# Kernel tuning notes

Hardware: AMD Instinct MI355X
Metric: run time of the kernel (lower is better)

Reference implementation:

```python
import jax, jax.numpy as jnp
import numpy as np

B, S, H = 2, 2048, 4096
NH, NKV, HD = 32, 8, 128
N_REP = NH // NKV
SCALING = HD ** -0.5


def rotate_half(x):
    x1, x2 = x[..., : HD // 2], x[..., HD // 2 :]
    return jnp.concatenate((-x2, x1), axis=-1)


def setup_inputs() -> dict:
    key = jax.random.key(0)
    ks = jax.random.split(key, 8)
    hidden_states = jax.random.normal(ks[0], (B, S, H), dtype=jnp.float32)
    # RoPE tables computed as in Llama (deterministic, realistic values)
    inv_freq = 1.0 / (10000.0 ** (jnp.arange(0, HD, 2, dtype=jnp.float32) / HD))
    t = jnp.arange(S, dtype=jnp.float32)
    freqs = jnp.einsum('s,d->sd', t, inv_freq)
    emb = jnp.concatenate((freqs, freqs), axis=-1)  # [S, HD]
    cos = jnp.broadcast_to(jnp.cos(emb)[None], (B, S, HD))
    sin = jnp.broadcast_to(jnp.sin(emb)[None], (B, S, HD))
    # additive causal mask [B,1,S,S]
    causal = jnp.where(jnp.tril(jnp.ones((S, S), dtype=bool)), 0.0, -1e9).astype(jnp.float32)
    attention_mask = jnp.broadcast_to(causal[None, None], (B, 1, S, S))
    std = 0.02
    Wq = jax.random.normal(ks[1], (NH * HD, H), dtype=jnp.float32) * std
    Wk = jax.random.normal(ks[2], (NKV * HD, H), dtype=jnp.float32) * std
    Wv = jax.random.normal(ks[3], (NKV * HD, H), dtype=jnp.float32) * std
    Wo = jax.random.normal(ks[4], (H, NH * HD), dtype=jnp.float32) * std
    return dict(hidden_states=hidden_states, cos=cos, sin=sin,
                attention_mask=attention_mask, Wq=Wq, Wk=Wk, Wv=Wv, Wo=Wo)


def reference(hidden_states, cos, sin, attention_mask, Wq, Wk, Wv, Wo):
    b, s, _ = hidden_states.shape
    # projections (torch Linear: x @ W.T), split into heads -> [B, nH, S, HD]
    q = (hidden_states @ Wq.T).reshape(b, s, NH, HD).transpose(0, 2, 1, 3)
    k = (hidden_states @ Wk.T).reshape(b, s, NKV, HD).transpose(0, 2, 1, 3)
    v = (hidden_states @ Wv.T).reshape(b, s, NKV, HD).transpose(0, 2, 1, 3)
    # RoPE: cos/sin [B,S,HD] -> [B,1,S,HD]
    c, sn = cos[:, None], sin[:, None]
    q = q * c + rotate_half(q) * sn
    k = k * c + rotate_half(k) * sn
    # GQA: repeat kv heads
    k = jnp.repeat(k, N_REP, axis=1)
    v = jnp.repeat(v, N_REP, axis=1)
    scores = jnp.einsum('bhqd,bhkd->bhqk', q, k) * SCALING + attention_mask
    attn = jax.nn.softmax(scores.astype(jnp.float32), axis=-1).astype(q.dtype)
    out = jnp.einsum('bhqk,bhkd->bhqd', attn, v)
    out = out.transpose(0, 2, 1, 3).reshape(b, s, NH * HD)
    return out @ Wo.T
```

## Files before the change

### kernel.cpp

```cpp
#include <hip/hip_runtime.h>
#include <stdint.h>

typedef unsigned short u16;
typedef __attribute__((ext_vector_type(8))) short short8;
typedef __attribute__((ext_vector_type(4))) float f32x4;
typedef __attribute__((ext_vector_type(16))) float f32x16;
typedef __attribute__((ext_vector_type(4))) u16 u16x4;

static constexpr float SCALE = 0.08838834764831845f;
static constexpr float QSCALE = 0.12752459769642898f;

__device__ __forceinline__ u16 f2bf(float f) {
    union { float f; unsigned u; } x; x.f = f;
    unsigned r = x.u + 0x7fffu + ((x.u >> 16) & 1u);
    return (u16)(r >> 16);
}
__device__ __forceinline__ float bf2f(u16 b) {
    union { unsigned u; float f; } x; x.u = ((unsigned)b) << 16;
    return x.f;
}
__device__ __forceinline__ unsigned cvt_pk_bf16(float lo, float hi_) {
    unsigned r;
    asm("v_cvt_pk_bf16_f32 %0, %1, %2" : "=v"(r) : "v"(lo), "v"(hi_));
    return r;
}

__global__ __launch_bounds__(256) void convert5_kernel(const float* __restrict__ s0, const float* __restrict__ s1,
                                                       const float* __restrict__ s2, const float* __restrict__ s3,
                                                       const float* __restrict__ s4,
                                                       u16* __restrict__ d0, u16* __restrict__ d1,
                                                       u16* __restrict__ d2, u16* __restrict__ d3,
                                                       u16* __restrict__ d4) {
    const int V0 = 4194304, V1 = 8388608, V2 = 9437184, V3 = 10485760, V4 = 14680064;
    const int stride = gridDim.x * blockDim.x;
    for (int i = blockIdx.x * blockDim.x + threadIdx.x; i < V4; i += stride) {
        const float* sp; u16* dp; int off;
        if (i < V0)      { sp = s0; dp = d0; off = i; }
        else if (i < V1) { sp = s1; dp = d1; off = i - V0; }
        else if (i < V2) { sp = s2; dp = d2; off = i - V1; }
        else if (i < V3) { sp = s3; dp = d3; off = i - V2; }
        else             { sp = s4; dp = d4; off = i - V3; }
        float4 v = *reinterpret_cast<const float4*>(sp + (size_t)off * 4);
        u16x4 o;
        o.x = f2bf(v.x); o.y = f2bf(v.y); o.z = f2bf(v.z); o.w = f2bf(v.w);
        *reinterpret_cast<u16x4*>(dp + (size_t)off * 4) = o;
    }
}

__global__ __launch_bounds__(256) void gemm_kv(const u16* __restrict__ A,
                                               const u16* __restrict__ Bk,
                                               const u16* __restrict__ Bv,
                                               u16* __restrict__ Ck,
                                               u16* __restrict__ Cvt) {
    constexpr int K = 4096, N = 1024, BK = 64;
    __shared__ u16 sA[128 * BK];
    __shared__ u16 sB[128 * BK];
    const int tid = threadIdx.x;
    const int wid = tid >> 6, lane = tid & 63;
    const int lrow = lane & 15, lgrp = lane >> 4;

    int bid = blockIdx.x;
    { const int cpx = 512 >> 3; bid = (bid & 7) * cpx + (bid >> 3); }
    const bool isV = bid >= 256;
    const int b2 = bid & 255;
    const int row0 = (b2 >> 3) * 128, col0 = (b2 & 7) * 128;
    const u16* __restrict__ B = isV ? Bv : Bk;
    const int wr = (wid >> 1) * 64, wc = (wid & 1) * 64;

    f32x4 acc[4][4] = {};

    const int NT = K / BK;
    for (int kt = 0; kt < NT; ++kt) {
        const int k0 = kt * BK;
        __syncthreads();
        #pragma unroll
        for (int rnd = 0; rnd < 4; ++rnd) {
            const int eoff = (rnd * 256 + tid) * 8;
            const int r = eoff >> 6, c = eoff & 63;
            const int gc = c ^ ((r & 7) << 3);
            const int ldsoff = rnd * 2048 + wid * 512;
            __builtin_amdgcn_global_load_lds(
                (const __attribute__((address_space(1))) void*)(A + (size_t)(row0 + r) * K + k0 + gc),
                (__attribute__((address_space(3))) void*)(&sA[ldsoff]), 16, 0, 0);
            __builtin_amdgcn_global_load_lds(
                (const __attribute__((address_space(1))) void*)(B + (size_t)(col0 + r) * K + k0 + gc),
                (__attribute__((address_space(3))) void*)(&sB[ldsoff]), 16, 0, 0);
        }
        __syncthreads();
        #pragma unroll
        for (int kk = 0; kk < 2; ++kk) {
            const int koff = kk * 32 + lgrp * 8;
            short8 af[4], bfr[4];
            #pragma unroll
            for (int m = 0; m < 4; ++m) {
                const int rr = wr + m * 16 + lrow;
                af[m] = *(const short8*)&sA[rr * BK + (koff ^ ((rr & 7) << 3))];
            }
            #pragma unroll
            for (int n = 0; n < 4; ++n) {
                const int rr = wc + n * 16 + lrow;
                bfr[n] = *(const short8*)&sB[rr * BK + (koff ^ ((rr & 7) << 3))];
            }
            #pragma unroll
            for (int m = 0; m < 4; ++m)
                #pragma unroll
                for (int n = 0; n < 4; ++n)
                    acc[m][n] = __builtin_amdgcn_mfma_f32_16x16x32_bf16(af[m], bfr[n], acc[m][n], 0, 0, 0);
        }
    }

    const int orow = row0 + wr + lgrp * 4;
    const int ocol = col0 + wc + lrow;
    if (!isV) {
        #pragma unroll
        for (int m = 0; m < 4; ++m)
            #pragma unroll
            for (int n = 0; n < 4; ++n)
                #pragma unroll
                for (int r = 0; r < 4; ++r)
                    Ck[(size_t)(orow + m * 16 + r) * N + ocol + n * 16] = f2bf(acc[m][n][r]);
    } else {
        #pragma unroll
        for (int m = 0; m < 4; ++m)
            #pragma unroll
            for (int n = 0; n < 4; ++n) {
                u16x4 pk;
                pk.x = f2bf(acc[m][n][0]); pk.y = f2bf(acc[m][n][1]);
                pk.z = f2bf(acc[m][n][2]); pk.w = f2bf(acc[m][n][3]);
                *(u16x4*)&Cvt[(size_t)(ocol + n * 16) * 4096 + orow + m * 16] = pk;
            }
    }
}

template<int OUT_MODE>
__global__ __launch_bounds__(512, 2) void gemm256v3(const u16* __restrict__ A,
                                                    const u16* __restrict__ B,
                                                    void* __restrict__ Cv,
                                                    int M, int N, int K) {
    __shared__ u16 sA[2][2][256 * 32];
    __shared__ u16 sB[2][2][256 * 32];
    const int tid = threadIdx.x;
    const int wid = tid >> 6, lane = tid & 63;
    const int lrow = lane & 15, lgrp = lane >> 4;

    const int nbn = N >> 8;
    const int total = (M >> 8) * nbn;
    int bid = blockIdx.x;
    if ((total & 7) == 0) { const int cpx = total >> 3; bid = (bid & 7) * cpx + (bid >> 3); }
    const int row0 = (bid / nbn) * 256, col0 = (bid % nbn) * 256;
    const int wr = (wid >> 2) * 128, wc = (wid & 3) * 64;

    f32x4 acc[8][4] = {};

    const int rS0 = wid * 32 + (lane >> 2);
    const int uS = lane & 3;

    auto stageA = [&](int nb, int kt, int kkh) {
        const int k0 = kt * 64 + kkh * 32;
        #pragma unroll
        for (int g = 0; g < 2; ++g) {
            const int r = rS0 + g * 16;
            const int cs = k0 + ((uS ^ ((r >> 1) & 3)) << 3);
            __builtin_amdgcn_global_load_lds(
                (const __attribute__((address_space(1))) void*)(A + (size_t)(row0 + r) * K + cs),
                (__attribute__((address_space(3))) void*)(&sA[nb][kkh][(wid * 32 + g * 16) * 32]), 16, 0, 0);
        }
    };
    auto stageB = [&](int nb, int kt, int kkh) {
        const int k0 = kt * 64 + kkh * 32;
        #pragma unroll
        for (int g = 0; g < 2; ++g) {
            const int r = rS0 + g * 16;
            const int cs = k0 + ((uS ^ ((r >> 1) & 3)) << 3);
            __builtin_amdgcn_global_load_lds(
                (const __attribute__((address_space(1))) void*)(B + (size_t)(col0 + r) * K + cs),
                (__attribute__((address_space(3))) void*)(&sB[nb][kkh][(wid * 32 + g * 16) * 32]), 16, 0, 0);
        }
    };

    auto rdA = [&](int buf, int kkh, int fr) -> short8 {
        const int r = wr + fr * 16 + lrow;
        return *(const short8*)&sA[buf][kkh][r * 32 + ((lgrp ^ ((r >> 1) & 3)) << 3)];
    };
    auto rdB = [&](int buf, int kkh, int fc) -> short8 {
        const int r = wc + fc * 16 + lrow;
        return *(const short8*)&sB[buf][kkh][r * 32 + ((lgrp ^ ((r >> 1) & 3)) << 3)];
    };

    const int NK = K >> 6;
    stageA(0, 0, 0); stageB(0, 0, 0); stageA(0, 0, 1); stageB(0, 0, 1);
    asm volatile("s_waitcnt vmcnt(4)" ::: "memory");
    __builtin_amdgcn_s_barrier();
    __builtin_amdgcn_sched_barrier(0);

    for (int kt = 0; kt < NK; ++kt) {
        const int buf = kt & 1, nb = buf ^ 1;
        const bool st = (kt + 1 < NK);
        short8 a[4], b[4], a2[4];

        #pragma unroll
        for (int fr = 0; fr < 4; ++fr) a[fr] = rdA(buf, 0, fr);
        #pragma unroll
        for (int fc = 0; fc < 4; ++fc) b[fc] = rdB(buf, 0, fc);
        if (st) stageA(nb, kt + 1, 0);
        asm volatile("s_waitcnt lgkmcnt(0)" ::: "memory");
        __builtin_amdgcn_sched_barrier(0);
        __builtin_amdgcn_s_setprio(1);
        #pragma unroll
        for (int fr = 0; fr < 4; ++fr)
            #pragma unroll
            for (int fc = 0; fc < 4; ++fc)
                acc[fr][fc] = __builtin_amdgcn_mfma_f32_16x16x32_bf16(a[fr], b[fc], acc[fr][fc], 0, 0, 0);
        __builtin_amdgcn_s_setprio(0);

        #pragma unroll
        for (int fr = 0; fr < 4; ++fr) a2[fr] = rdA(buf, 0, fr + 4);
        if (st) stageB(nb, kt + 1, 0);
        asm volatile("s_waitcnt lgkmcnt(0)" ::: "memory");
        __builtin_amdgcn_sched_barrier(0);
        __builtin_amdgcn_s_setprio(1);
        #pragma unroll
        for (int fr = 0; fr < 4; ++fr)
            #pragma unroll
            for (int fc = 0; fc < 4; ++fc)
                acc[fr + 4][fc] = __builtin_amdgcn_mfma_f32_16x16x32_bf16(a2[fr], b[fc], acc[fr + 4][fc], 0, 0, 0);
        __builtin_amdgcn_s_setprio(0);
        if (st) { asm volatile("s_waitcnt vmcnt(4)" ::: "memory"); }
        else    { asm volatile("s_waitcnt vmcnt(0)" ::: "memory"); }
        __builtin_amdgcn_s_barrier();
        __builtin_amdgcn_sched_barrier(0);

        #pragma unroll
        for (int fr = 0; fr < 4; ++fr) a[fr] = rdA(buf, 1, fr);
        #pragma unroll
        for (int fc = 0; fc < 4; ++fc) b[fc] = rdB(buf, 1, fc);
        if (st) stageA(nb, kt + 1, 1);
        asm volatile("s_waitcnt lgkmcnt(0)" ::: "memory");
        __builtin_amdgcn_sched_barrier(0);
        __builtin_amdgcn_s_setprio(1);
        #pragma unroll
        for (int fr = 0; fr < 4; ++fr)
            #pragma unroll
            for (int fc = 0; fc < 4; ++fc)
                acc[fr][fc] = __builtin_amdgcn_mfma_f32_16x16x32_bf16(a[fr], b[fc], acc[fr][fc], 0, 0, 0);
        __builtin_amdgcn_s_setprio(0);

        #pragma unroll
        for (int fr = 0; fr < 4; ++fr) a2[fr] = rdA(buf, 1, fr + 4);
        if (st) stageB(nb, kt + 1, 1);
        asm volatile("s_waitcnt lgkmcnt(0)" ::: "memory");
        __builtin_amdgcn_sched_barrier(0);
        __builtin_amdgcn_s_setprio(1);
        #pragma unroll
        for (int fr = 0; fr < 4; ++fr)
            #pragma unroll
            for (int fc = 0; fc < 4; ++fc)
                acc[fr + 4][fc] = __builtin_amdgcn_mfma_f32_16x16x32_bf16(a2[fr], b[fc], acc[fr + 4][fc], 0, 0, 0);
        __builtin_amdgcn_s_setprio(0);
        if (st) { asm volatile("s_waitcnt vmcnt(4)" ::: "memory"); }
        __builtin_amdgcn_s_barrier();
        __builtin_amdgcn_sched_barrier(0);
    }

    const int orow = row0 + wr + lgrp * 4;
    const int ocol = col0 + wc + lrow;
    if (OUT_MODE == 2) {
        float* C = (float*)Cv;
        #pragma unroll
        for (int m = 0; m < 8; ++m)
            #pragma unroll
            for (int n = 0; n < 4; ++n)
                #pragma unroll
                for (int r = 0; r < 4; ++r)
                    C[(size_t)(orow + m * 16 + r) * N + ocol + n * 16] = acc[m][n][r];
    } else {
        u16* C = (u16*)Cv;
        #pragma unroll
        for (int m = 0; m < 8; ++m)
            #pragma unroll
            for (int n = 0; n < 4; ++n)
                #pragma unroll
                for (int r = 0; r < 4; ++r)
                    C[(size_t)(orow + m * 16 + r) * N + ocol + n * 16] = f2bf(acc[m][n][r]);
    }
}

template<int NHEADS>
__global__ __launch_bounds__(256) void rope_kernel(u16* __restrict__ X,
                                                   const float* __restrict__ cosb,
                                                   const float* __restrict__ sinb,
                                                   float scale) {
    constexpr int LH = (NHEADS == 32) ? 5 : 3;
    const int total = 2 * 2048 * NHEADS * 64;
    const int stride = gridDim.x * blockDim.x;
    for (int i = blockIdx.x * blockDim.x + threadIdx.x; i < total; i += stride) {
        const int d = i & 63;
        const int h = (i >> 6) & (NHEADS - 1);
        const int rs = i >> (6 + LH);
        const size_t base = (size_t)rs * (NHEADS * 128) + h * 128 + d;
        const float c = cosb[rs * 128 + d] * scale;
        const float sn = sinb[rs * 128 + d] * scale;
        const float x1 = bf2f(X[base]);
        const float x2 = bf2f(X[base + 64]);
        X[base] = f2bf(x1 * c - x2 * sn);
        X[base + 64] = f2bf(x2 * c + x1 * sn);
    }
}

__global__ __launch_bounds__(512, 2) void attn_kernel(const u16* __restrict__ Q,
                                                      const u16* __restrict__ K,
                                                      const u16* __restrict__ Vt,
                                                      u16* __restrict__ AO,
                                                      const float* __restrict__ cosp,
                                                      const float* __restrict__ sinp) {
    __shared__ u16 sK[2][64 * 128];
    __shared__ u16 sV[2][128 * 64];
    const int tid = threadIdx.x;
    const int wid = tid >> 6, lane = tid & 63;
    const int l31 = lane & 31, hi = lane >> 5;

    const int gg = blockIdx.x >> 6;
    const int bx = (gg < 4) ? gg : 11 - gg;
    const int rem = blockIdx.x & 63;
    const int h = rem >> 1;
    const int b = rem & 1;
    const int hkv = h >> 2;
    const int rs0 = b * 2048;
    const int q0 = bx * 256;
    const int qw = q0 + wid * 32;
    const int q_lane = qw + l31;

    short8 qf[8];
    {
        const u16* qb = Q + (size_t)(rs0 + q_lane) * 4096 + h * 128 + hi * 8;
        #pragma unroll
        for (int f = 0; f < 8; ++f) qf[f] = *(const short8*)(qb + f * 16);
        const float* cb = cosp + (size_t)(rs0 + q_lane) * 128 + hi * 8;
        const float* sb = sinp + (size_t)(rs0 + q_lane) * 128 + hi * 8;
        #pragma unroll
        for (int f = 0; f < 4; ++f) {
            float4 c0 = *(const float4*)(cb + f * 16);
            float4 c1 = *(const float4*)(cb + f * 16 + 4);
            float4 s0 = *(const float4*)(sb + f * 16);
            float4 s1 = *(const float4*)(sb + f * 16 + 4);
            const float cc[8] = {c0.x, c0.y, c0.z, c0.w, c1.x, c1.y, c1.z, c1.w};
            const float ss[8] = {s0.x, s0.y, s0.z, s0.w, s1.x, s1.y, s1.z, s1.w};
            #pragma unroll
            for (int jj = 0; jj < 8; ++jj) {
                const float x1 = bf2f((u16)qf[f][jj]);
                const float x2 = bf2f((u16)qf[f + 4][jj]);
                qf[f][jj]     = (short)f2bf((x1 * cc[jj] - x2 * ss[jj]) * QSCALE);
                qf[f + 4][jj] = (short)f2bf((x2 * cc[jj] + x1 * ss[jj]) * QSCALE);
            }
        }
    }

    f32x16 accO[4] = {};
    float m_c = -1e30f, l_c = 0.f;

    auto stage = [&](int bf, int t) {
        const int kv0 = t * 64;
        #pragma unroll
        for (int rnd = 0; rnd < 2; ++rnd) {
            {
                const int e = rnd * 4096 + tid * 8;
                const int r = e >> 7, c = e & 127;
                const int cs = c ^ ((r & 15) << 3);
                __builtin_amdgcn_global_load_lds(
                    (const __attribute__((address_space(1))) void*)(K + (size_t)(rs0 + kv0 + r) * 1024 + hkv * 128 + cs),
                    (__attribute__((address_space(3))) void*)(&sK[bf][rnd * 4096 + wid * 512]), 16, 0, 0);
            }
            {
                const int e = rnd * 4096 + tid * 8;
                const int r = e >> 6, c = e & 63;
                const int cs = c ^ ((r & 7) << 3);
                __builtin_amdgcn_global_load_lds(
                    (const __attribute__((address_space(1))) void*)(Vt + (size_t)(hkv * 128 + r) * 4096 + rs0 + kv0 + cs),
                    (__attribute__((address_space(3))) void*)(&sV[bf][rnd * 4096 + wid * 512]), 16, 0, 0);
            }
        }
    };

    const int NT = 4 * (bx + 1);
    stage(0, 0);
    __syncthreads();
    int buf = 0;

    for (int t = 0; t < NT; ++t) {
        if (t + 1 < NT) stage(buf ^ 1, t + 1);
        const int kv0 = t * 64;

        if (kv0 <= qw + 31) {
            f32x16 sc[2] = {};
            #pragma unroll
            for (int f = 0; f < 8; ++f) {
                const int col = f * 16 + hi * 8;
                const int r0 = l31, r1 = 32 + l31;
                short8 k0 = *(const short8*)&sK[buf][r0 * 128 + (col ^ ((r0 & 15) << 3))];
                short8 k1 = *(const short8*)&sK[buf][r1 * 128 + (col ^ ((r1 & 15) << 3))];
                sc[0] = __builtin_amdgcn_mfma_f32_32x32x16_bf16(k0, qf[f], sc[0], 0, 0, 0);
                sc[1] = __builtin_amdgcn_mfma_f32_32x32x16_bf16(k1, qf[f], sc[1], 0, 0, 0);
            }

            if (kv0 + 63 > q_lane) {
                #pragma unroll
                for (int blk = 0; blk < 2; ++blk)
                    #pragma unroll
                    for (int r = 0; r < 16; ++r) {
                        const int kv_abs = kv0 + blk * 32 + ((r & 3) + 8 * (r >> 2) + 4 * hi);
                        if (kv_abs > q_lane) sc[blk][r] = -1e30f;
                    }
            }

            float mx = sc[0][0];
            #pragma unroll
            for (int blk = 0; blk < 2; ++blk)
                #pragma unroll
                for (int r = 0; r < 16; ++r) mx = fmaxf(mx, sc[blk][r]);
            mx = fmaxf(mx, __shfl_xor(mx, 32));

            if (!__all(mx <= m_c + 8.0f)) {
                const float sclf = __builtin_amdgcn_exp2f(m_c - mx);
                m_c = mx;
                l_c *= sclf;
                float sclq[16];
                #pragma unroll
                for (int r = 0; r < 16; ++r)
                    sclq[r] = __shfl(sclf, (r & 3) + 8 * (r >> 2) + 4 * hi);
                #pragma unroll
                for (int d4 = 0; d4 < 4; ++d4)
                    #pragma unroll
                    for (int r = 0; r < 16; ++r) accO[d4][r] *= sclq[r];
            }
            float ssum = 0.f;
            #pragma unroll
            for (int blk = 0; blk < 2; ++blk)
                #pragma unroll
                for (int r = 0; r < 16; ++r) {
                    const float p = __builtin_amdgcn_exp2f(sc[blk][r] - m_c);
                    sc[blk][r] = p;
                    ssum += p;
                }
            ssum += __shfl_xor(ssum, 32);
            l_c += ssum;

            #pragma unroll
            for (int blk = 0; blk < 2; ++blk) {
                #pragma unroll
                for (int tt = 0; tt < 2; ++tt) {
                    const unsigned cv00 = cvt_pk_bf16(sc[blk][8 * tt + 0], sc[blk][8 * tt + 1]);
                    const unsigned cv01 = cvt_pk_bf16(sc[blk][8 * tt + 2], sc[blk][8 * tt + 3]);
                    const unsigned cv10 = cvt_pk_bf16(sc[blk][8 * tt + 4], sc[blk][8 * tt + 5]);
                    const unsigned cv11 = cvt_pk_bf16(sc[blk][8 * tt + 6], sc[blk][8 * tt + 7]);
                    const unsigned s00 = __shfl_xor(cv00, 32);
                    const unsigned s01 = __shfl_xor(cv01, 32);
                    const unsigned s10 = __shfl_xor(cv10, 32);
                    const unsigned s11 = __shfl_xor(cv11, 32);
                    union { unsigned w[4]; short8 v; } pa;
                    pa.w[0] = hi ? s10 : cv00;
                    pa.w[1] = hi ? s11 : cv01;
                    pa.w[2] = hi ? cv10 : s00;
                    pa.w[3] = hi ? cv11 : s01;
                    const int kvb = blk * 32 + tt * 16 + hi * 8;
                    #pragma unroll
                    for (int d4 = 0; d4 < 4; ++d4) {
                        const int vr = d4 * 32 + l31;
                        short8 vf = *(const short8*)&sV[buf][vr * 64 + (kvb ^ ((vr & 7) << 3))];
                        accO[d4] = __builtin_amdgcn_mfma_f32_32x32x16_bf16(pa.v, vf, accO[d4], 0, 0, 0);
                    }
                }
            }
        }
        __syncthreads();
        buf ^= 1;
    }

    const float invl = 1.0f / l_c;
    float invq[16];
    #pragma unroll
    for (int r = 0; r < 16; ++r)
        invq[r] = __shfl(invl, (r & 3) + 8 * (r >> 2) + 4 * hi);
    #pragma unroll
    for (int d4 = 0; d4 < 4; ++d4)
        #pragma unroll
        for (int r = 0; r < 16; ++r) {
            const int q = qw + (r & 3) + 8 * (r >> 2) + 4 * hi;
            AO[(size_t)(rs0 + q) * 4096 + h * 128 + d4 * 32 + l31] = f2bf(accO[d4][r] * invq[r]);
        }
}

extern "C" void kernel_launch(void* const* d_in, const int* in_sizes, int n_in,
                              void* d_out, int out_size, void* d_ws, size_t ws_size,
                              hipStream_t stream) {
    const float* hs   = (const float*)d_in[0];
    const float* cosp = (const float*)d_in[1];
    const float* sinp = (const float*)d_in[2];
    const float* Wq = (const float*)d_in[4];
    const float* Wk = (const float*)d_in[5];
    const float* Wv = (const float*)d_in[6];
    const float* Wo = (const float*)d_in[7];

    u16* Xb = (u16*)d_out;
    u16* Qb = (u16*)d_out + 16777216;
    char* w = (char*)d_ws;
    u16* Wqb = (u16*)w; w += 33554432;
    u16* Wkb = (u16*)w; w += 8388608;
    u16* Wvb = (u16*)w; w += 8388608;
    u16* Wob = (u16*)w; w += 33554432;
    u16* Kb  = (u16*)w; w += 8388608;
    u16* Vtb = (u16*)w; w += 8388608;
    u16* AOb = (u16*)w; w += 33554432;

    convert5_kernel<<<4096, 256, 0, stream>>>(hs, Wq, Wk, Wv, Wo, Xb, Wqb, Wkb, Wvb, Wob);

    gemm256v3<0><<<256, 512, 0, stream>>>(Xb, Wqb, Qb, 4096, 4096, 4096);
    gemm_kv<<<512, 256, 0, stream>>>(Xb, Wkb, Wvb, Kb, Vtb);

    rope_kernel<8><<<1024, 256, 0, stream>>>(Kb, cosp, sinp, 1.0f);

    attn_kernel<<<512, 512, 0, stream>>>(Qb, Kb, Vtb, AOb, cosp, sinp);

    gemm256v3<2><<<256, 512, 0, stream>>>(AOb, Wob, (float*)d_out, 4096, 4096, 4096);
}
```

Before: 523.8 us.

## Software-pipeline LDS fragment reads across MFMA phases in 256x256 GEMM

Restructures the GEMM main loop so the LDS fragment loads for the next MFMA block are issued before the current block's MFMAs run. Partial lgkmcnt waits let the matrix instructions overlap shared-memory reads, and the first fragments of the next k-tile are prefetched after the barrier. Launch bounds drop to one 512-thread block per CU so the extra fragment registers fit, at the cost of lower occupancy for the Q and output projections.

```diff
diff --git a/kernel.cpp b/kernel.cpp
--- a/kernel.cpp
+++ b/kernel.cpp
@@ -133,7 +133,7 @@
 }
 
 template<int OUT_MODE>
-__global__ __launch_bounds__(512, 2) void gemm256v3(const u16* __restrict__ A,
+__global__ __launch_bounds__(512, 1) void gemm256v5(const u16* __restrict__ A,
                                                     const u16* __restrict__ B,
                                                     void* __restrict__ Cv,
                                                     int M, int N, int K) {
@@ -193,72 +193,86 @@
     __builtin_amdgcn_s_barrier();
     __builtin_amdgcn_sched_barrier(0);
 
+    short8 a0[4], b0[4], a1[4], a2[4], b1[4], a3[4];
+    #pragma unroll
+    for (int fr = 0; fr < 4; ++fr) a0[fr] = rdA(0, 0, fr);
+    #pragma unroll
+    for (int fc = 0; fc < 4; ++fc) b0[fc] = rdB(0, 0, fc);
+    __builtin_amdgcn_sched_barrier(0);
+
     for (int kt = 0; kt < NK; ++kt) {
         const int buf = kt & 1, nb = buf ^ 1;
         const bool st = (kt + 1 < NK);
-        short8 a[4], b[4], a2[4];
-
-        #pragma unroll
-        for (int fr = 0; fr < 4; ++fr) a[fr] = rdA(buf, 0, fr);
-        #pragma unroll
-        for (int fc = 0; fc < 4; ++fc) b[fc] = rdB(buf, 0, fc);
+
+        #pragma unroll
+        for (int fr = 0; fr < 4; ++fr) a1[fr] = rdA(buf, 0, fr + 4);
         if (st) stageA(nb, kt + 1, 0);
-        asm volatile("s_waitcnt lgkmcnt(0)" ::: "memory");
+        asm volatile("s_waitcnt lgkmcnt(4)" ::: "memory");
         __builtin_amdgcn_sched_barrier(0);
         __builtin_amdgcn_s_setprio(1);
         #pragma unroll
         for (int fr = 0; fr < 4; ++fr)
             #pragma unroll
             for (int fc = 0; fc < 4; ++fc)
-                acc[fr][fc] = __builtin_amdgcn_mfma_f32_16x16x32_bf16(a[fr], b[fc], acc[fr][fc], 0, 0, 0);
+                acc[fr][fc] = __builtin_amdgcn_mfma_f32_16x16x32_bf16(a0[fr], b0[fc], acc[fr][fc], 0, 0, 0);
         __builtin_amdgcn_s_setprio(0);
-
-        #pragma unroll
-        for (int fr = 0; fr < 4; ++fr) a2[fr] = rdA(buf, 0, fr + 4);
+        __builtin_amdgcn_sched_barrier(0);
+
         if (st) stageB(nb, kt + 1, 0);
         asm volatile("s_waitcnt lgkmcnt(0)" ::: "memory");
         __builtin_amdgcn_sched_barrier(0);
-        __builtin_amdgcn_s_setprio(1);
-        #pragma unroll
-        for (int fr = 0; fr < 4; ++fr)
-            #pragma unroll
-            for (int fc = 0; fc < 4; ++fc)
-                acc[fr + 4][fc] = __builtin_amdgcn_mfma_f32_16x16x32_bf16(a2[fr], b[fc], acc[fr + 4][fc], 0, 0, 0);
-        __builtin_amdgcn_s_setprio(0);
         if (st) { asm volatile("s_waitcnt vmcnt(4)" ::: "memory"); }
         else    { asm volatile("s_waitcnt vmcnt(0)" ::: "memory"); }
         __builtin_amdgcn_s_barrier();
         __builtin_amdgcn_sched_barrier(0);
-
-        #pragma unroll
-        for (int fr = 0; fr < 4; ++fr) a[fr] = rdA(buf, 1, fr);
-        #pragma unroll
-        for (int fc = 0; fc < 4; ++fc) b[fc] = rdB(buf, 1, fc);
+        #pragma unroll
+        for (int fr = 0; fr < 4; ++fr) a2[fr] = rdA(buf, 1, fr);
+        #pragma unroll
+        for (int fc = 0; fc < 4; ++fc) b1[fc] = rdB(buf, 1, fc);
+        __builtin_amdgcn_sched_barrier(0);
+        __builtin_amdgcn_s_setprio(1);
+        #pragma unroll
+        for (int fr = 0; fr < 4; ++fr)
+            #pragma unroll
+            for (int fc = 0; fc < 4; ++fc)
+                acc[fr + 4][fc] = __builtin_amdgcn_mfma_f32_16x16x32_bf16(a1[fr], b0[fc], acc[fr + 4][fc], 0, 0, 0);
+        __builtin_amdgcn_s_setprio(0);
+        __builtin_amdgcn_sched_barrier(0);
+
+        #pragma unroll
+        for (int fr = 0; fr < 4; ++fr) a3[fr] = rdA(buf, 1, fr + 4);
         if (st) stageA(nb, kt + 1, 1);
-        asm volatile("s_waitcnt lgkmcnt(0)" ::: "memory");
+        asm volatile("s_waitcnt lgkmcnt(4)" ::: "memory");
         __builtin_amdgcn_sched_barrier(0);
         __builtin_amdgcn_s_setprio(1);
         #pragma unroll
         for (int fr = 0; fr < 4; ++fr)
             #pragma unroll
             for (int fc = 0; fc < 4; ++fc)
-                acc[fr][fc] = __builtin_amdgcn_mfma_f32_16x16x32_bf16(a[fr], b[fc], acc[fr][fc], 0, 0, 0);
+                acc[fr][fc] = __builtin_amdgcn_mfma_f32_16x16x32_bf16(a2[fr], b1[fc], acc[fr][fc], 0, 0, 0);
         __builtin_amdgcn_s_setprio(0);
-
-        #pragma unroll
-        for (int fr = 0; fr < 4; ++fr) a2[fr] = rdA(buf, 1, fr + 4);
+        __builtin_amdgcn_sched_barrier(0);
+
         if (st) stageB(nb, kt + 1, 1);
         asm volatile("s_waitcnt lgkmcnt(0)" ::: "memory");
         __builtin_amdgcn_sched_barrier(0);
-        __builtin_amdgcn_s_setprio(1);
-        #pragma unroll
-        for (int fr = 0; fr < 4; ++fr)
-            #pragma unroll
-            for (int fc = 0; fc < 4; ++fc)
-                acc[fr + 4][fc] = __builtin_amdgcn_mfma_f32_16x16x32_bf16(a2[fr], b[fc], acc[fr + 4][fc], 0, 0, 0);
-        __builtin_amdgcn_s_setprio(0);
         if (st) { asm volatile("s_waitcnt vmcnt(4)" ::: "memory"); }
         __builtin_amdgcn_s_barrier();
+        __builtin_amdgcn_sched_barrier(0);
+        if (st) {
+            #pragma unroll
+            for (int fr = 0; fr < 4; ++fr) a0[fr] = rdA(nb, 0, fr);
+            #pragma unroll
+            for (int fc = 0; fc < 4; ++fc) b0[fc] = rdB(nb, 0, fc);
+        }
+        __builtin_amdgcn_sched_barrier(0);
+        __builtin_amdgcn_s_setprio(1);
+        #pragma unroll
+        for (int fr = 0; fr < 4; ++fr)
+            #pragma unroll
+            for (int fc = 0; fc < 4; ++fc)
+                acc[fr + 4][fc] = __builtin_amdgcn_mfma_f32_16x16x32_bf16(a3[fr], b1[fc], acc[fr + 4][fc], 0, 0, 0);
+        __builtin_amdgcn_s_setprio(0);
         __builtin_amdgcn_sched_barrier(0);
     }
 
@@ -513,12 +527,12 @@
 
     convert5_kernel<<<4096, 256, 0, stream>>>(hs, Wq, Wk, Wv, Wo, Xb, Wqb, Wkb, Wvb, Wob);
 
-    gemm256v3<0><<<256, 512, 0, stream>>>(Xb, Wqb, Qb, 4096, 4096, 4096);
+    gemm256v5<0><<<256, 512, 0, stream>>>(Xb, Wqb, Qb, 4096, 4096, 4096);
     gemm_kv<<<512, 256, 0, stream>>>(Xb, Wkb, Wvb, Kb, Vtb);
 
     rope_kernel<8><<<1024, 256, 0, stream>>>(Kb, cosp, sinp, 1.0f);
 
     attn_kernel<<<512, 512, 0, stream>>>(Qb, Kb, Vtb, AOb, cosp, sinp);
 
-    gemm256v3<2><<<256, 512, 0, stream>>>(AOb, Wob, (float*)d_out, 4096, 4096, 4096);
-}
+    gemm256v5<2><<<256, 512, 0, stream>>>(AOb, Wob, (float*)d_out, 4096, 4096, 4096);
+}
```

New measurement: 502.4 us, median of 3. 1.04x faster.

## Rewrite 256x256 GEMM with 16 waves and a simpler double-buffered loop

Applied to the files above, without the earlier changes.

Replaces the 8-wave 256x256-tile GEMM with a 16-wave (1024-thread) variant. Each wave now owns a 64x64 subtile with a 4x4 accumulator instead of 128x64. The hand-scheduled interleaving of LDS reads, async global-to-LDS staging and explicit waitcnt is replaced by one stage-next-then-compute loop with a __syncthreads per k-step. The aim is more waves for latency hiding and less register pressure. The cost is losing the fine-grained overlap and the two-blocks-per-CU occupancy, and each wave reads more LDS per MFMA.

```diff
diff --git a/kernel.cpp b/kernel.cpp
--- a/kernel.cpp
+++ b/kernel.cpp
@@ -133,10 +133,10 @@
 }
 
 template<int OUT_MODE>
-__global__ __launch_bounds__(512, 2) void gemm256v3(const u16* __restrict__ A,
-                                                    const u16* __restrict__ B,
-                                                    void* __restrict__ Cv,
-                                                    int M, int N, int K) {
+__global__ __launch_bounds__(1024, 1) void gemm16w(const u16* __restrict__ A,
+                                                   const u16* __restrict__ B,
+                                                   void* __restrict__ Cv,
+                                                   int M, int N, int K) {
     __shared__ u16 sA[2][2][256 * 32];
     __shared__ u16 sB[2][2][256 * 32];
     const int tid = threadIdx.x;
@@ -148,118 +148,58 @@
     int bid = blockIdx.x;
     if ((total & 7) == 0) { const int cpx = total >> 3; bid = (bid & 7) * cpx + (bid >> 3); }
     const int row0 = (bid / nbn) * 256, col0 = (bid % nbn) * 256;
-    const int wr = (wid >> 2) * 128, wc = (wid & 3) * 64;
-
-    f32x4 acc[8][4] = {};
-
-    const int rS0 = wid * 32 + (lane >> 2);
-    const int uS = lane & 3;
-
-    auto stageA = [&](int nb, int kt, int kkh) {
-        const int k0 = kt * 64 + kkh * 32;
-        #pragma unroll
-        for (int g = 0; g < 2; ++g) {
-            const int r = rS0 + g * 16;
-            const int cs = k0 + ((uS ^ ((r >> 1) & 3)) << 3);
+    const int wr = (wid >> 2) * 64, wc = (wid & 3) * 64;
+
+    f32x4 acc[4][4] = {};
+
+    const int rS = tid >> 2;
+    const int uS = tid & 3;
+    const int sOff = wid * 512;
+
+    auto stage = [&](int nb, int kt) {
+        #pragma unroll
+        for (int kkh = 0; kkh < 2; ++kkh) {
+            const int k0 = kt * 64 + kkh * 32;
+            const int cs = k0 + ((uS ^ ((rS >> 1) & 3)) << 3);
             __builtin_amdgcn_global_load_lds(
-                (const __attribute__((address_space(1))) void*)(A + (size_t)(row0 + r) * K + cs),
-                (__attribute__((address_space(3))) void*)(&sA[nb][kkh][(wid * 32 + g * 16) * 32]), 16, 0, 0);
+                (const __attribute__((address_space(1))) void*)(A + (size_t)(row0 + rS) * K + cs),
+                (__attribute__((address_space(3))) void*)(&sA[nb][kkh][sOff]), 16, 0, 0);
+            __builtin_amdgcn_global_load_lds(
+                (const __attribute__((address_space(1))) void*)(B + (size_t)(col0 + rS) * K + cs),
+                (__attribute__((address_space(3))) void*)(&sB[nb][kkh][sOff]), 16, 0, 0);
         }
     };
-    auto stageB = [&](int nb, int kt, int kkh) {
-        const int k0 = kt * 64 + kkh * 32;
-        #pragma unroll
-        for (int g = 0; g < 2; ++g) {
-            const int r = rS0 + g * 16;
-            const int cs = k0 + ((uS ^ ((r >> 1) & 3)) << 3);
-            __builtin_amdgcn_global_load_lds(
-                (const __attribute__((address_space(1))) void*)(B + (size_t)(col0 + r) * K + cs),
-                (__attribute__((address_space(3))) void*)(&sB[nb][kkh][(wid * 32 + g * 16) * 32]), 16, 0, 0);
-        }
-    };
-
-    auto rdA = [&](int buf, int kkh, int fr) -> short8 {
-        const int r = wr + fr * 16 + lrow;
-        return *(const short8*)&sA[buf][kkh][r * 32 + ((lgrp ^ ((r >> 1) & 3)) << 3)];
-    };
-    auto rdB = [&](int buf, int kkh, int fc) -> short8 {
-        const int r = wc + fc * 16 + lrow;
-        return *(const short8*)&sB[buf][kkh][r * 32 + ((lgrp ^ ((r >> 1) & 3)) << 3)];
-    };
 
     const int NK = K >> 6;
-    stageA(0, 0, 0); stageB(0, 0, 0); stageA(0, 0, 1); stageB(0, 0, 1);
-    asm volatile("s_waitcnt vmcnt(4)" ::: "memory");
-    __builtin_amdgcn_s_barrier();
-    __builtin_amdgcn_sched_barrier(0);
+    stage(0, 0);
+    __syncthreads();
 
     for (int kt = 0; kt < NK; ++kt) {
-        const int buf = kt & 1, nb = buf ^ 1;
-        const bool st = (kt + 1 < NK);
-        short8 a[4], b[4], a2[4];
-
-        #pragma unroll
-        for (int fr = 0; fr < 4; ++fr) a[fr] = rdA(buf, 0, fr);
-        #pragma unroll
-        for (int fc = 0; fc < 4; ++fc) b[fc] = rdB(buf, 0, fc);
-        if (st) stageA(nb, kt + 1, 0);
-        asm volatile("s_waitcnt lgkmcnt(0)" ::: "memory");
-        __builtin_amdgcn_sched_barrier(0);
-        __builtin_amdgcn_s_setprio(1);
-        #pragma unroll
-        for (int fr = 0; fr < 4; ++fr)
-            #pragma unroll
-            for (int fc = 0; fc < 4; ++fc)
-                acc[fr][fc] = __builtin_amdgcn_mfma_f32_16x16x32_bf16(a[fr], b[fc], acc[fr][fc], 0, 0, 0);
-        __builtin_amdgcn_s_setprio(0);
-
-        #pragma unroll
-        for (int fr = 0; fr < 4; ++fr) a2[fr] = rdA(buf, 0, fr + 4);
-        if (st) stageB(nb, kt + 1, 0);
-        asm volatile("s_waitcnt lgkmcnt(0)" ::: "memory");
-        __builtin_amdgcn_sched_barrier(0);
-        __builtin_amdgcn_s_setprio(1);
-        #pragma unroll
-        for (int fr = 0; fr < 4; ++fr)
-            #pragma unroll
-            for (int fc = 0; fc < 4; ++fc)
-                acc[fr + 4][fc] = __builtin_amdgcn_mfma_f32_16x16x32_bf16(a2[fr], b[fc], acc[fr + 4][fc], 0, 0, 0);
-        __builtin_amdgcn_s_setprio(0);
-        if (st) { asm volatile("s_waitcnt vmcnt(4)" ::: "memory"); }
-        else    { asm volatile("s_waitcnt vmcnt(0)" ::: "memory"); }
-        __builtin_amdgcn_s_barrier();
-        __builtin_amdgcn_sched_barrier(0);
-
-        #pragma unroll
-        for (int fr = 0; fr < 4; ++fr) a[fr] = rdA(buf, 1, fr);
-        #pragma unroll
-        for (int fc = 0; fc < 4; ++fc) b[fc] = rdB(buf, 1, fc);
-        if (st) stageA(nb, kt + 1, 1);
-        asm volatile("s_waitcnt lgkmcnt(0)" ::: "memory");
-        __builtin_amdgcn_sched_barrier(0);
-        __builtin_amdgcn_s_setprio(1);
-        #pragma unroll
-        for (int fr = 0; fr < 4; ++fr)
-            #pragma unroll
-            for (int fc = 0; fc < 4; ++fc)
-                acc[fr][fc] = __builtin_amdgcn_mfma_f32_16x16x32_bf16(a[fr], b[fc], acc[fr][fc], 0, 0, 0);
-        __builtin_amdgcn_s_setprio(0);
-
-        #pragma unroll
-        for (int fr = 0; fr < 4; ++fr) a2[fr] = rdA(buf, 1, fr + 4);
-        if (st) stageB(nb, kt + 1, 1);
-        asm volatile("s_waitcnt lgkmcnt(0)" ::: "memory");
-        __builtin_amdgcn_sched_barrier(0);
-        __builtin_amdgcn_s_setprio(1);
-        #pragma unroll
-        for (int fr = 0; fr < 4; ++fr)
-            #pragma unroll
-            for (int fc = 0; fc < 4; ++fc)
-                acc[fr + 4][fc] = __builtin_amdgcn_mfma_f32_16x16x32_bf16(a2[fr], b[fc], acc[fr + 4][fc], 0, 0, 0);
-        __builtin_amdgcn_s_setprio(0);
-        if (st) { asm volatile("s_waitcnt vmcnt(4)" ::: "memory"); }
-        __builtin_amdgcn_s_barrier();
-        __builtin_amdgcn_sched_barrier(0);
+        const int buf = kt & 1;
+        if (kt + 1 < NK) stage(buf ^ 1, kt + 1);
+
+        #pragma unroll
+        for (int kkh = 0; kkh < 2; ++kkh) {
+            short8 a[4], b[4];
+            #pragma unroll
+            for (int fr = 0; fr < 4; ++fr) {
+                const int r = wr + fr * 16 + lrow;
+                a[fr] = *(const short8*)&sA[buf][kkh][r * 32 + ((lgrp ^ ((r >> 1) & 3)) << 3)];
+            }
+            #pragma unroll
+            for (int fc = 0; fc < 4; ++fc) {
+                const int r = wc + fc * 16 + lrow;
+                b[fc] = *(const short8*)&sB[buf][kkh][r * 32 + ((lgrp ^ ((r >> 1) & 3)) << 3)];
+            }
+            __builtin_amdgcn_s_setprio(1);
+            #pragma unroll
+            for (int fr = 0; fr < 4; ++fr)
+                #pragma unroll
+                for (int fc = 0; fc < 4; ++fc)
+                    acc[fr][fc] = __builtin_amdgcn_mfma_f32_16x16x32_bf16(a[fr], b[fc], acc[fr][fc], 0, 0, 0);
+            __builtin_amdgcn_s_setprio(0);
+        }
+        __syncthreads();
     }
 
     const int orow = row0 + wr + lgrp * 4;
@@ -267,7 +207,7 @@
     if (OUT_MODE == 2) {
         float* C = (float*)Cv;
         #pragma unroll
-        for (int m = 0; m < 8; ++m)
+        for (int m = 0; m < 4; ++m)
             #pragma unroll
             for (int n = 0; n < 4; ++n)
                 #pragma unroll
@@ -276,7 +216,7 @@
     } else {
         u16* C = (u16*)Cv;
         #pragma unroll
-        for (int m = 0; m < 8; ++m)
+        for (int m = 0; m < 4; ++m)
             #pragma unroll
             for (int n = 0; n < 4; ++n)
                 #pragma unroll
@@ -513,12 +453,12 @@
 
     convert5_kernel<<<4096, 256, 0, stream>>>(hs, Wq, Wk, Wv, Wo, Xb, Wqb, Wkb, Wvb, Wob);
 
-    gemm256v3<0><<<256, 512, 0, stream>>>(Xb, Wqb, Qb, 4096, 4096, 4096);
+    gemm16w<0><<<256, 1024, 0, stream>>>(Xb, Wqb, Qb, 4096, 4096, 4096);
     gemm_kv<<<512, 256, 0, stream>>>(Xb, Wkb, Wvb, Kb, Vtb);
 
     rope_kernel<8><<<1024, 256, 0, stream>>>(Kb, cosp, sinp, 1.0f);
 
     attn_kernel<<<512, 512, 0, stream>>>(Qb, Kb, Vtb, AOb, cosp, sinp);
 
-    gemm256v3<2><<<256, 512, 0, stream>>>(AOb, Wob, (float*)d_out, 4096, 4096, 4096);
-}
+    gemm16w<2><<<256, 1024, 0, stream>>>(AOb, Wob, (float*)d_out, 4096, 4096, 4096);
+}
```

New measurement: 509.3 us. 1.03x faster.

## Restructure 256x256 GEMM into 3-stage LDS ring with register prefetch

Applied to the files above, without the earlier changes.

Rewrites the main GEMM loop to use a three-slot ring of 32-wide K tiles in LDS instead of a double-buffered pair of 64-wide tiles. Global loads are issued two tiles ahead, and the next tile's A/B fragments are loaded into registers before the second MFMA half runs, so LDS reads overlap with matrix math. This cuts the barrier count per K step and deepens latency hiding. In exchange it uses more registers (launch bounds lowered to 1 block per 2 waves-per-EU hint) and a more intricate waitcnt scheme.

```diff
diff --git a/kernel.cpp b/kernel.cpp
--- a/kernel.cpp
+++ b/kernel.cpp
@@ -133,12 +133,12 @@
 }
 
 template<int OUT_MODE>
-__global__ __launch_bounds__(512, 2) void gemm256v3(const u16* __restrict__ A,
+__global__ __launch_bounds__(512, 1) void gemm256v6(const u16* __restrict__ A,
                                                     const u16* __restrict__ B,
                                                     void* __restrict__ Cv,
                                                     int M, int N, int K) {
-    __shared__ u16 sA[2][2][256 * 32];
-    __shared__ u16 sB[2][2][256 * 32];
+    __shared__ u16 sA[3][256 * 32];
+    __shared__ u16 sB[3][256 * 32];
     const int tid = threadIdx.x;
     const int wid = tid >> 6, lane = tid & 63;
     const int lrow = lane & 15, lgrp = lane >> 4;
@@ -155,111 +155,97 @@
     const int rS0 = wid * 32 + (lane >> 2);
     const int uS = lane & 3;
 
-    auto stageA = [&](int nb, int kt, int kkh) {
-        const int k0 = kt * 64 + kkh * 32;
+    auto stageA = [&](int s, int kt) {
+        const int k0 = kt * 32;
         #pragma unroll
         for (int g = 0; g < 2; ++g) {
             const int r = rS0 + g * 16;
             const int cs = k0 + ((uS ^ ((r >> 1) & 3)) << 3);
             __builtin_amdgcn_global_load_lds(
                 (const __attribute__((address_space(1))) void*)(A + (size_t)(row0 + r) * K + cs),
-                (__attribute__((address_space(3))) void*)(&sA[nb][kkh][(wid * 32 + g * 16) * 32]), 16, 0, 0);
+                (__attribute__((address_space(3))) void*)(&sA[s][(wid * 32 + g * 16) * 32]), 16, 0, 0);
         }
     };
-    auto stageB = [&](int nb, int kt, int kkh) {
-        const int k0 = kt * 64 + kkh * 32;
+    auto stageB = [&](int s, int kt) {
+        const int k0 = kt * 32;
         #pragma unroll
         for (int g = 0; g < 2; ++g) {
             const int r = rS0 + g * 16;
             const int cs = k0 + ((uS ^ ((r >> 1) & 3)) << 3);
             __builtin_amdgcn_global_load_lds(
                 (const __attribute__((address_space(1))) void*)(B + (size_t)(col0 + r) * K + cs),
-                (__attribute__((address_space(3))) void*)(&sB[nb][kkh][(wid * 32 + g * 16) * 32]), 16, 0, 0);
+                (__attribute__((address_space(3))) void*)(&sB[s][(wid * 32 + g * 16) * 32]), 16, 0, 0);
         }
     };
 
-    auto rdA = [&](int buf, int kkh, int fr) -> short8 {
+    auto rdA = [&](int s, int fr) -> short8 {
         const int r = wr + fr * 16 + lrow;
-        return *(const short8*)&sA[buf][kkh][r * 32 + ((lgrp ^ ((r >> 1) & 3)) << 3)];
+        return *(const short8*)&sA[s][r * 32 + ((lgrp ^ ((r >> 1) & 3)) << 3)];
     };
-    auto rdB = [&](int buf, int kkh, int fc) -> short8 {
+    auto rdB = [&](int s, int fc) -> short8 {
         const int r = wc + fc * 16 + lrow;
-        return *(const short8*)&sB[buf][kkh][r * 32 + ((lgrp ^ ((r >> 1) & 3)) << 3)];
+        return *(const short8*)&sB[s][r * 32 + ((lgrp ^ ((r >> 1) & 3)) << 3)];
     };
 
-    const int NK = K >> 6;
-    stageA(0, 0, 0); stageB(0, 0, 0); stageA(0, 0, 1); stageB(0, 0, 1);
+    const int NK = K >> 5;
+    stageA(0, 0); stageB(0, 0); stageA(1, 1); stageB(1, 1);
     asm volatile("s_waitcnt vmcnt(4)" ::: "memory");
     __builtin_amdgcn_s_barrier();
     __builtin_amdgcn_sched_barrier(0);
 
-    for (int kt = 0; kt < NK; ++kt) {
-        const int buf = kt & 1, nb = buf ^ 1;
-        const bool st = (kt + 1 < NK);
-        short8 a[4], b[4], a2[4];
-
-        #pragma unroll
-        for (int fr = 0; fr < 4; ++fr) a[fr] = rdA(buf, 0, fr);
-        #pragma unroll
-        for (int fc = 0; fc < 4; ++fc) b[fc] = rdB(buf, 0, fc);
-        if (st) stageA(nb, kt + 1, 0);
+    short8 A0[4], B0[4], A1[4], B1[4], ah[4];
+    #pragma unroll
+    for (int fr = 0; fr < 4; ++fr) A0[fr] = rdA(0, fr);
+    #pragma unroll
+    for (int fc = 0; fc < 4; ++fc) B0[fc] = rdB(0, fc);
+    __builtin_amdgcn_sched_barrier(0);
+
+    auto tile = [&](int t, short8 (&cal)[4], short8 (&cbb)[4], short8 (&nal)[4], short8 (&nbb)[4]) {
+        const int bt = t % 3;
+        const bool st = (t + 2 < NK);
+
+        #pragma unroll
+        for (int fr = 0; fr < 4; ++fr) ah[fr] = rdA(bt, fr + 4);
+        if (st) stageA((t + 2) % 3, t + 2);
+        asm volatile("s_waitcnt lgkmcnt(4)" ::: "memory");
+        __builtin_amdgcn_sched_barrier(0);
+        __builtin_amdgcn_s_setprio(1);
+        #pragma unroll
+        for (int fr = 0; fr < 4; ++fr)
+            #pragma unroll
+            for (int fc = 0; fc < 4; ++fc)
+                acc[fr][fc] = __builtin_amdgcn_mfma_f32_16x16x32_bf16(cal[fr], cbb[fc], acc[fr][fc], 0, 0, 0);
+        __builtin_amdgcn_s_setprio(0);
+        __builtin_amdgcn_sched_barrier(0);
+
+        if (st) stageB((t + 2) % 3, t + 2);
         asm volatile("s_waitcnt lgkmcnt(0)" ::: "memory");
         __builtin_amdgcn_sched_barrier(0);
-        __builtin_amdgcn_s_setprio(1);
-        #pragma unroll
-        for (int fr = 0; fr < 4; ++fr)
-            #pragma unroll
-            for (int fc = 0; fc < 4; ++fc)
-                acc[fr][fc] = __builtin_amdgcn_mfma_f32_16x16x32_bf16(a[fr], b[fc], acc[fr][fc], 0, 0, 0);
-        __builtin_amdgcn_s_setprio(0);
-
-        #pragma unroll
-        for (int fr = 0; fr < 4; ++fr) a2[fr] = rdA(buf, 0, fr + 4);
-        if (st) stageB(nb, kt + 1, 0);
-        asm volatile("s_waitcnt lgkmcnt(0)" ::: "memory");
+        if (t < NK - 2) { asm volatile("s_waitcnt vmcnt(4)" ::: "memory"); }
+        else            { asm volatile("s_waitcnt vmcnt(0)" ::: "memory"); }
+        __builtin_amdgcn_s_barrier();
+        __builtin_amdgcn_sched_barrier(0);
+        if (t + 1 < NK) {
+            const int bn = (t + 1) % 3;
+            #pragma unroll
+            for (int fr = 0; fr < 4; ++fr) nal[fr] = rdA(bn, fr);
+            #pragma unroll
+            for (int fc = 0; fc < 4; ++fc) nbb[fc] = rdB(bn, fc);
+        }
         __builtin_amdgcn_sched_barrier(0);
         __builtin_amdgcn_s_setprio(1);
         #pragma unroll
         for (int fr = 0; fr < 4; ++fr)
             #pragma unroll
             for (int fc = 0; fc < 4; ++fc)
-                acc[fr + 4][fc] = __builtin_amdgcn_mfma_f32_16x16x32_bf16(a2[fr], b[fc], acc[fr + 4][fc], 0, 0, 0);
+                acc[fr + 4][fc] = __builtin_amdgcn_mfma_f32_16x16x32_bf16(ah[fr], cbb[fc], acc[fr + 4][fc], 0, 0, 0);
         __builtin_amdgcn_s_setprio(0);
-        if (st) { asm volatile("s_waitcnt vmcnt(4)" ::: "memory"); }
-        else    { asm volatile("s_waitcnt vmcnt(0)" ::: "memory"); }
-        __builtin_amdgcn_s_barrier();
         __builtin_amdgcn_sched_barrier(0);
-
-        #pragma unroll
-        for (int fr = 0; fr < 4; ++fr) a[fr] = rdA(buf, 1, fr);
-        #pragma unroll
-        for (int fc = 0; fc < 4; ++fc) b[fc] = rdB(buf, 1, fc);
-        if (st) stageA(nb, kt + 1, 1);
-        asm volatile("s_waitcnt lgkmcnt(0)" ::: "memory");
-        __builtin_amdgcn_sched_barrier(0);
-        __builtin_amdgcn_s_setprio(1);
-        #pragma unroll
-        for (int fr = 0; fr < 4; ++fr)
-            #pragma unroll
-            for (int fc = 0; fc < 4; ++fc)
-                acc[fr][fc] = __builtin_amdgcn_mfma_f32_16x16x32_bf16(a[fr], b[fc], acc[fr][fc], 0, 0, 0);
-        __builtin_amdgcn_s_setprio(0);
-
-        #pragma unroll
-        for (int fr = 0; fr < 4; ++fr) a2[fr] = rdA(buf, 1, fr + 4);
-        if (st) stageB(nb, kt + 1, 1);
-        asm volatile("s_waitcnt lgkmcnt(0)" ::: "memory");
-        __builtin_amdgcn_sched_barrier(0);
-        __builtin_amdgcn_s_setprio(1);
-        #pragma unroll
-        for (int fr = 0; fr < 4; ++fr)
-            #pragma unroll
-            for (int fc = 0; fc < 4; ++fc)
-                acc[fr + 4][fc] = __builtin_amdgcn_mfma_f32_16x16x32_bf16(a2[fr], b[fc], acc[fr + 4][fc], 0, 0, 0);
-        __builtin_amdgcn_s_setprio(0);
-        if (st) { asm volatile("s_waitcnt vmcnt(4)" ::: "memory"); }
-        __builtin_amdgcn_s_barrier();
-        __builtin_amdgcn_sched_barrier(0);
+    };
+
+    for (int t = 0; t < NK; t += 2) {
+        tile(t, A0, B0, A1, B1);
+        tile(t + 1, A1, B1, A0, B0);
     }
 
     const int orow = row0 + wr + lgrp * 4;
@@ -513,12 +499,12 @@
 
     convert5_kernel<<<4096, 256, 0, stream>>>(hs, Wq, Wk, Wv, Wo, Xb, Wqb, Wkb, Wvb, Wob);
 
-    gemm256v3<0><<<256, 512, 0, stream>>>(Xb, Wqb, Qb, 4096, 4096, 4096);
+    gemm256v6<0><<<256, 512, 0, stream>>>(Xb, Wqb, Qb, 4096, 4096, 4096);
     gemm_kv<<<512, 256, 0, stream>>>(Xb, Wkb, Wvb, Kb, Vtb);
 
     rope_kernel<8><<<1024, 256, 0, stream>>>(Kb, cosp, sinp, 1.0f);
 
     attn_kernel<<<512, 512, 0, stream>>>(Qb, Kb, Vtb, AOb, cosp, sinp);
 
-    gemm256v3<2><<<256, 512, 0, stream>>>(AOb, Wob, (float*)d_out, 4096, 4096, 4096);
-}
+    gemm256v6<2><<<256, 512, 0, stream>>>(AOb, Wob, (float*)d_out, 4096, 4096, 4096);
+}
```

Result: no change. 523.2 us (-0.1%).
